# Performance work log

Hardware: AMD Instinct MI355X
Metric: run time of the kernel (lower is better)

Reference implementation:

```python
import jax, jax.numpy as jnp
import numpy as np

B, L, D = 2, 2048, 2048
H, G, E = 16, 4, 128       # num_heads, group_num, head dim
KV = H // G                # kv heads = 4
OUT = D                    # output_dim == input_dim for residual


def setup_inputs() -> dict:
    key = jax.random.key(0)
    ks = jax.random.split(key, 12)
    s_in = 1.0 / np.sqrt(D)
    s_o = 1.0 / np.sqrt(H * E)
    return {
        "x": jax.random.normal(ks[0], (B, L, D), jnp.float32),
        "Wq": jax.random.normal(ks[1], (D, H * E), jnp.float32) * s_in,
        "bq": jnp.zeros((H * E,), jnp.float32),
        "Wk": jax.random.normal(ks[2], (D, KV * E), jnp.float32) * s_in,
        "bk": jnp.zeros((KV * E,), jnp.float32),
        "Wv": jax.random.normal(ks[3], (D, KV * E), jnp.float32) * s_in,
        "bv": jnp.zeros((KV * E,), jnp.float32),
        "Wo": jax.random.normal(ks[4], (H * E, OUT), jnp.float32) * s_o,
        "bo": jnp.zeros((OUT,), jnp.float32),
        "gamma": jnp.ones((OUT,), jnp.float32),
        "beta": jnp.zeros((OUT,), jnp.float32),
    }


def reference(x, Wq, bq, Wk, bk, Wv, bv, Wo, bo, gamma, beta):
    b, l, _ = x.shape
    Q = (x @ Wq + bq).reshape(b, l, H, E)            # [B,L,H,E]
    K = (x @ Wk + bk).reshape(b, l, KV, E)           # [B,L,KV,E]
    V = (x @ Wv + bv).reshape(b, l, KV, E)
    # GQA expand: reshape(B,L,1,KV,E).expand(G) -> head h = g*KV + kv (tile kv heads G times)
    K = jnp.broadcast_to(K[:, :, None, :, :], (b, l, G, KV, E)).reshape(b, l, H, E)
    V = jnp.broadcast_to(V[:, :, None, :, :], (b, l, G, KV, E)).reshape(b, l, H, E)
    scores = jnp.einsum('blhe,bmhe->bhlm', Q, K) / np.sqrt(E).astype(np.float32)
    # causal mask: triu(ones, diag=1) * -1e9 added to scores
    mask = jnp.triu(jnp.ones((l, l), jnp.float32), k=1) * (-1e9)
    attn = jax.nn.softmax(scores + mask[None, None, :, :], axis=-1)
    ctx = jnp.einsum('bhlm,bmhe->blhe', attn, V).reshape(b, l, H * E)
    y = jax.nn.gelu(ctx @ Wo + bo, approximate=False)  # nn.GELU default = exact erf
    r = x + y
    mu = jnp.mean(r, axis=-1, keepdims=True)
    var = jnp.var(r, axis=-1, keepdims=True)
    return (r - mu) * jax.lax.rsqrt(var + 1e-5) * gamma + beta
```

## Files before the change

### kernel.cpp

```cpp
#include <hip/hip_runtime.h>
#include <hip/hip_bf16.h>
#include <math.h>

typedef __bf16 bf16_t;
typedef __bf16 bf16x4 __attribute__((ext_vector_type(4)));
typedef __bf16 bf16x8 __attribute__((ext_vector_type(8)));
typedef float  f32x4  __attribute__((ext_vector_type(4)));
typedef float  f32x16 __attribute__((ext_vector_type(16)));

#define MFMA16(a,b,c) __builtin_amdgcn_mfma_f32_16x16x32_bf16((a),(b),(c),0,0,0)
#define MFMA32(a,b,c) __builtin_amdgcn_mfma_f32_32x32x16_bf16((a),(b),(c),0,0,0)

#define B_ 2
#define L_ 2048
#define D_ 2048
#define H_ 16
#define KV_ 4
#define E_ 128
#define M_ (B_*L_)
#define NQKV_ 3072

__device__ __forceinline__ void async_ld16(const bf16_t* g, bf16_t* l) {
    __builtin_amdgcn_global_load_lds((const __attribute__((address_space(1))) void*)g,
                                     (__attribute__((address_space(3))) void*)l, 16, 0, 0);
}

__global__ __launch_bounds__(256) void cast_bias_kernel(const float* __restrict__ src,
                                                        bf16_t* __restrict__ dst,
                                                        const float* __restrict__ bq,
                                                        const float* __restrict__ bk,
                                                        const float* __restrict__ bv,
                                                        float* __restrict__ qbias) {
    int bid = blockIdx.x;
    if (bid < 8192) {
        int i = (bid * 256 + threadIdx.x) * 4;
        float4 v = *(const float4*)(src + i);
        bf16x4 o;
        o.x = (bf16_t)v.x; o.y = (bf16_t)v.y; o.z = (bf16_t)v.z; o.w = (bf16_t)v.w;
        *(bf16x4*)(dst + i) = o;
    } else {
        int i = (bid - 8192) * 256 + threadIdx.x;
        if (i < 2048) qbias[i] = bq[i];
        else if (i < 2560) qbias[i] = bk[i - 2048];
        else if (i < 3072) qbias[i] = bv[i - 2560];
    }
}

__global__ __launch_bounds__(256) void wtrans_kernel(const float* __restrict__ Wq,
                                                     const float* __restrict__ Wk,
                                                     const float* __restrict__ Wv,
                                                     const float* __restrict__ Wo,
                                                     bf16_t* __restrict__ WqkvT,
                                                     bf16_t* __restrict__ WoT) {
    __shared__ float tile[32][33];
    int bx = blockIdx.x;
    const float* W; bf16_t* WT; int N, n0;
    if (bx < 64)      { W = Wq; WT = WqkvT;                  N = 2048; n0 = bx * 32; }
    else if (bx < 80) { W = Wk; WT = WqkvT + 2048 * 2048;    N = 512;  n0 = (bx - 64) * 32; }
    else if (bx < 96) { W = Wv; WT = WqkvT + 2560 * 2048;    N = 512;  n0 = (bx - 80) * 32; }
    else              { W = Wo; WT = WoT;                    N = 2048; n0 = (bx - 96) * 32; }
    int k0 = blockIdx.y * 32;
    int tx = threadIdx.x, ty = threadIdx.y;
    #pragma unroll
    for (int i = 0; i < 32; i += 8)
        tile[ty + i][tx] = W[(size_t)(k0 + ty + i) * N + n0 + tx];
    __syncthreads();
    #pragma unroll
    for (int i = 0; i < 32; i += 8)
        WT[(size_t)(n0 + ty + i) * 2048 + k0 + tx] = (bf16_t)tile[tx][ty + i];
}

__global__ __launch_bounds__(256) void transpose_v_kernel(const bf16_t* __restrict__ QKV,
                                                          bf16_t* __restrict__ Vt) {
    __shared__ bf16_t tile[32][33];
    int e0 = blockIdx.x * 32, l0 = blockIdx.y * 32;
    int bk = blockIdx.z;
    int b = bk >> 2, kv = bk & 3;
    int tx = threadIdx.x, ty = threadIdx.y;
    #pragma unroll
    for (int i = 0; i < 32; i += 8)
        tile[ty + i][tx] = QKV[(size_t)(b * L_ + l0 + ty + i) * NQKV_ + 2560 + kv * 128 + e0 + tx];
    __syncthreads();
    #pragma unroll
    for (int i = 0; i < 32; i += 8)
        Vt[((size_t)bk * 128 + e0 + ty + i) * L_ + l0 + tx] = tile[tx][ty + i];
}

template <bool OUT_BF16, bool GELU>
__global__ __launch_bounds__(256) void gemm_kernel(const bf16_t* __restrict__ A,
                                                   const bf16_t* __restrict__ BT,
                                                   const float* __restrict__ bias,
                                                   void* __restrict__ C,
                                                   int M, int N, int K) {
    __shared__ __align__(16) bf16_t sA[128][32];
    __shared__ __align__(16) bf16_t sB[128][32];
    int tid = threadIdx.x;
    int wave = tid >> 6, lane = tid & 63;
    int l16 = lane & 15, quad = lane >> 4;
    int row0 = blockIdx.y * 128;
    int col0 = blockIdx.x * 128;
    int wm = (wave >> 1) * 64;
    int wn = (wave & 1) * 64;

    f32x4 acc[4][4];
    #pragma unroll
    for (int i = 0; i < 4; ++i)
        #pragma unroll
        for (int j = 0; j < 4; ++j)
            acc[i][j] = f32x4{0.f, 0.f, 0.f, 0.f};

    for (int k0 = 0; k0 < K; k0 += 32) {
        #pragma unroll
        for (int c = 0; c < 2; ++c) {
            int lin = (c * 256 + tid) * 8;
            int r = lin >> 5, col = lin & 31;
            async_ld16(&A[(size_t)(row0 + r) * K + k0 + col], &sA[r][col]);
            async_ld16(&BT[(size_t)(col0 + r) * K + k0 + col], &sB[r][col]);
        }
        __syncthreads();
        bf16x8 af[4], bf[4];
        #pragma unroll
        for (int mt = 0; mt < 4; ++mt) af[mt] = *(const bf16x8*)&sA[wm + mt * 16 + l16][quad * 8];
        #pragma unroll
        for (int nt = 0; nt < 4; ++nt) bf[nt] = *(const bf16x8*)&sB[wn + nt * 16 + l16][quad * 8];
        #pragma unroll
        for (int mt = 0; mt < 4; ++mt)
            #pragma unroll
            for (int nt = 0; nt < 4; ++nt)
                acc[mt][nt] = MFMA16(af[mt], bf[nt], acc[mt][nt]);
        __syncthreads();
    }

    #pragma unroll
    for (int mt = 0; mt < 4; ++mt) {
        #pragma unroll
        for (int nt = 0; nt < 4; ++nt) {
            int gcol = col0 + wn + nt * 16 + l16;
            float bv = bias[gcol];
            #pragma unroll
            for (int r = 0; r < 4; ++r) {
                int grow = row0 + wm + mt * 16 + quad * 4 + r;
                float v = acc[mt][nt][r] + bv;
                if (GELU) v = 0.5f * v * (1.f + erff(v * 0.70710678118654752f));
                if (OUT_BF16) ((bf16_t*)C)[(size_t)grow * N + gcol] = (bf16_t)v;
                else          ((float*)C)[(size_t)grow * N + gcol] = v;
            }
        }
    }
}

__global__ __launch_bounds__(128, 2) void attn_kernel(const bf16_t* __restrict__ QKV,
                                                      const bf16_t* __restrict__ Vt,
                                                      bf16_t* __restrict__ Ctx) {
    __shared__ __align__(16) bf16_t sK[2][64][128];

    const int tid = threadIdx.x;
    const int wave = tid >> 6, lane = tid & 63;
    const int l31 = lane & 31, half = lane >> 5;

    const int idx = blockIdx.x;
    const int rr = idx >> 5;
    const int bh = idx & 31;
    const int u = (rr < 8) ? 31 - rr : (rr < 16) ? rr - 8 : (rr < 24) ? 39 - rr : rr - 16;
    const int h = bh & 15, b = bh >> 4;
    const int kv = h & 3;

    const bf16_t* Kbase = QKV + (size_t)b * L_ * NQKV_ + 2048 + kv * 128;
    const bf16_t* Vbase = Vt + (size_t)(b * 4 + kv) * 128 * L_;
    const float SC = 0.12754995f;

    const int qrow = u * 64 + wave * 32 + l31;

    bf16x8 qf[8];
    const bf16_t* Qrow = QKV + (size_t)(b * L_ + qrow) * NQKV_ + h * 128 + half * 8;
    #pragma unroll
    for (int et = 0; et < 8; ++et) qf[et] = *(const bf16x8*)&Qrow[et * 16];

    f32x16 acc[4];
    #pragma unroll
    for (int em = 0; em < 4; ++em)
        #pragma unroll
        for (int j = 0; j < 16; ++j) acc[em][j] = 0.f;
    float l_i = 0.f;

    #define STAGE_K(KT, BUF)                                                          \
        {                                                                             \
            int kk = (KT) * 64;                                                       \
            _Pragma("unroll")                                                         \
            for (int rep = 0; rep < 8; ++rep) {                                       \
                int ch = rep * 128 + tid;                                             \
                int rk = ch >> 4;                                                     \
                int sc = (ch & 15) ^ (rk & 15);                                       \
                async_ld16(&Kbase[(size_t)(kk + rk) * NQKV_ + sc * 8],                \
                           ((bf16_t*)sK[BUF]) + (size_t)ch * 8);                      \
            }                                                                         \
        }

    STAGE_K(0, 0);
    __syncthreads();

    for (int kt = 0; kt <= u; ++kt) {
        const int bufi = kt & 1;
        if (kt < u) STAGE_K(kt + 1, bufi ^ 1);

        bf16x8 vr[16];
        #pragma unroll
        for (int kc = 0; kc < 2; ++kc)
            #pragma unroll
            for (int em = 0; em < 4; ++em)
                vr[kc * 4 + em] = *(const bf16x8*)&Vbase[(size_t)(em * 32 + l31) * L_ +
                                                         kt * 64 + (kc * 2 + half) * 8];

        f32x16 s[2];
        #pragma unroll
        for (int mt = 0; mt < 2; ++mt)
            #pragma unroll
            for (int j = 0; j < 16; ++j) s[mt][j] = 0.f;
        __builtin_amdgcn_s_setprio(1);
        #pragma unroll
        for (int mt = 0; mt < 2; ++mt)
            #pragma unroll
            for (int et = 0; et < 8; ++et) {
                bf16x8 kf = *(const bf16x8*)&sK[bufi][mt * 32 + l31][((et * 2 + half) ^ (l31 & 15)) * 8];
                s[mt] = MFMA32(kf, qf[et], s[mt]);
            }
        __builtin_amdgcn_s_setprio(0);

        #pragma unroll
        for (int kc = 2; kc < 4; ++kc)
            #pragma unroll
            for (int em = 0; em < 4; ++em)
                vr[kc * 4 + em] = *(const bf16x8*)&Vbase[(size_t)(em * 32 + l31) * L_ +
                                                         kt * 64 + (kc * 2 + half) * 8];

        if (kt == u) {
            #pragma unroll
            for (int mt = 0; mt < 2; ++mt)
                #pragma unroll
                for (int j = 0; j < 16; ++j) {
                    int kidx = kt * 64 + mt * 32 + (j & 3) + 8 * (j >> 2) + 4 * half;
                    if (kidx > qrow) s[mt][j] = -3.0e38f;
                }
        }

        float rs = 0.f;
        #pragma unroll
        for (int mt = 0; mt < 2; ++mt)
            #pragma unroll
            for (int j = 0; j < 16; ++j) {
                float p = exp2f(s[mt][j] * SC);
                s[mt][j] = p;
                rs += p;
            }
        rs += __shfl_xor(rs, 32, 64);
        l_i += rs;

        bf16x4 pk[2][4];
        #pragma unroll
        for (int mt = 0; mt < 2; ++mt)
            #pragma unroll
            for (int g = 0; g < 4; ++g) {
                bf16x4 tt;
                #pragma unroll
                for (int i = 0; i < 4; ++i) tt[i] = (bf16_t)s[mt][g * 4 + i];
                pk[mt][g] = tt;
            }

        #pragma unroll
        for (int kc = 0; kc < 4; ++kc) {
            const int mts = kc >> 1, g0 = 2 * (kc & 1);
            bf16x4 send = half ? pk[mts][g0] : pk[mts][g0 + 1];
            bf16x4 keep = half ? pk[mts][g0 + 1] : pk[mts][g0];
            union { bf16x4 v; int i[2]; } su, ru;
            su.v = send;
            ru.i[0] = __shfl_xor(su.i[0], 32, 64);
            ru.i[1] = __shfl_xor(su.i[1], 32, 64);
            bf16x4 lo = half ? ru.v : keep;
            bf16x4 hi = half ? keep : ru.v;
            bf16x8 pf = __builtin_shufflevector(lo, hi, 0, 1, 2, 3, 4, 5, 6, 7);
            __builtin_amdgcn_s_setprio(1);
            #pragma unroll
            for (int em = 0; em < 4; ++em)
                acc[em] = MFMA32(vr[kc * 4 + em], pf, acc[em]);
            __builtin_amdgcn_s_setprio(0);
        }

        __syncthreads();
    }

    const float inv = 1.f / l_i;
    bf16_t* Cp = Ctx + (size_t)(b * L_ + qrow) * 2048 + h * 128;
    #pragma unroll
    for (int em = 0; em < 4; ++em)
        #pragma unroll
        for (int g = 0; g < 4; ++g) {
            bf16x4 ov;
            #pragma unroll
            for (int i = 0; i < 4; ++i) ov[i] = (bf16_t)(acc[em][g * 4 + i] * inv);
            *(bf16x4*)&Cp[em * 32 + g * 8 + half * 4] = ov;
        }
}

__global__ __launch_bounds__(256) void ln_kernel(const bf16_t* __restrict__ Y,
                                                 const float* __restrict__ X,
                                                 const float* __restrict__ gamma,
                                                 const float* __restrict__ beta,
                                                 float* __restrict__ out) {
    __shared__ float sr[2048];
    __shared__ float wred[8];
    size_t row = blockIdx.x;
    const bf16_t* y = Y + row * 2048;
    const float* x = X + row * 2048;
    float sum = 0.f, ssq = 0.f;
    #pragma unroll
    for (int c = 0; c < 2; ++c) {
        int i = (c * 256 + threadIdx.x) * 4;
        bf16x4 yv = *(const bf16x4*)(y + i);
        float4 xv = *(const float4*)(x + i);
        float r0 = xv.x + (float)yv[0];
        float r1 = xv.y + (float)yv[1];
        float r2 = xv.z + (float)yv[2];
        float r3 = xv.w + (float)yv[3];
        sr[i] = r0; sr[i + 1] = r1; sr[i + 2] = r2; sr[i + 3] = r3;
        sum += r0 + r1 + r2 + r3;
        ssq += r0 * r0 + r1 * r1 + r2 * r2 + r3 * r3;
    }
    #pragma unroll
    for (int off = 32; off > 0; off >>= 1) {
        sum += __shfl_xor(sum, off, 64);
        ssq += __shfl_xor(ssq, off, 64);
    }
    int wv = threadIdx.x >> 6;
    if ((threadIdx.x & 63) == 0) { wred[wv] = sum; wred[wv + 4] = ssq; }
    __syncthreads();
    sum = wred[0] + wred[1] + wred[2] + wred[3];
    ssq = wred[4] + wred[5] + wred[6] + wred[7];
    float mu = sum * (1.f / 2048.f);
    float var = ssq * (1.f / 2048.f) - mu * mu;
    float rstd = rsqrtf(var + 1e-5f);
    #pragma unroll
    for (int c = 0; c < 2; ++c) {
        int i = (c * 256 + threadIdx.x) * 4;
        float4 gv = *(const float4*)(gamma + i);
        float4 bv = *(const float4*)(beta + i);
        float4 o;
        o.x = (sr[i]     - mu) * rstd * gv.x + bv.x;
        o.y = (sr[i + 1] - mu) * rstd * gv.y + bv.y;
        o.z = (sr[i + 2] - mu) * rstd * gv.z + bv.z;
        o.w = (sr[i + 3] - mu) * rstd * gv.w + bv.w;
        *(float4*)(out + row * 2048 + i) = o;
    }
}

extern "C" void kernel_launch(void* const* d_in, const int* in_sizes, int n_in,
                              void* d_out, int out_size, void* d_ws, size_t ws_size,
                              hipStream_t stream) {
    const float* x     = (const float*)d_in[0];
    const float* Wq    = (const float*)d_in[1];
    const float* bq    = (const float*)d_in[2];
    const float* Wk    = (const float*)d_in[3];
    const float* bk    = (const float*)d_in[4];
    const float* Wv    = (const float*)d_in[5];
    const float* bv    = (const float*)d_in[6];
    const float* Wo    = (const float*)d_in[7];
    const float* bo    = (const float*)d_in[8];
    const float* gamma = (const float*)d_in[9];
    const float* beta  = (const float*)d_in[10];
    float* out = (float*)d_out;

    char* ws = (char*)d_ws;
    size_t off = 0;
    bf16_t* xb    = (bf16_t*)(ws + off); off += 16777216;
    bf16_t* WqkvT = (bf16_t*)(ws + off); off += 12582912;
    bf16_t* WoT   = (bf16_t*)(ws + off); off += 8388608;
    float*  qbias = (float*)(ws + off);  off += 12288;
    bf16_t* QKV   = (bf16_t*)(ws + off); off += 25165824;
    bf16_t* Vt    = (bf16_t*)(ws + off); off += 4194304;
    bf16_t* Cb    = (bf16_t*)(ws + off); off += 16777216;
    bf16_t* Yb    = (bf16_t*)(ws + off); off += 16777216;

    cast_bias_kernel<<<8204, 256, 0, stream>>>(x, xb, bq, bk, bv, qbias);
    wtrans_kernel<<<dim3(160, 64), dim3(32, 8), 0, stream>>>(Wq, Wk, Wv, Wo, WqkvT, WoT);

    gemm_kernel<true, false><<<dim3(24, 32), 256, 0, stream>>>(xb, WqkvT, qbias, QKV, M_, NQKV_, D_);
    transpose_v_kernel<<<dim3(4, 64, 8), dim3(32, 8), 0, stream>>>(QKV, Vt);
    attn_kernel<<<1024, 128, 0, stream>>>(QKV, Vt, Cb);
    gemm_kernel<true, true><<<dim3(16, 32), 256, 0, stream>>>(Cb, WoT, bo, Yb, M_, D_, 2048);
    ln_kernel<<<M_, 256, 0, stream>>>(Yb, x, gamma, beta, out);
}
```

Measured before the change: 358.7 us.

## Split attention KV loop across two wave pairs and merge partials via LDS

The attention block grows to 256 threads. Two wave pairs process alternating 64-key tiles for the same 64 query rows, each with its own double-buffered K staging. Their unnormalized accumulators and row sums are combined through shared memory at the end. This works because the softmax has no running max, so the partials can simply be added. The block order becomes a plain longest-first schedule, exp2f becomes the hardware intrinsic, and the row sum is split into four partial sums. The aim is to shorten the serial KV loop per block and improve latency hiding, at the cost of more LDS, a final reduction step, and idle waves on odd tile counts.

```diff
diff --git a/kernel.cpp b/kernel.cpp
--- a/kernel.cpp
+++ b/kernel.cpp
@@ -149,19 +149,20 @@
     }
 }
 
-__global__ __launch_bounds__(128, 2) void attn_kernel(const bf16_t* __restrict__ QKV,
+__global__ __launch_bounds__(256, 2) void attn_kernel(const bf16_t* __restrict__ QKV,
                                                       const bf16_t* __restrict__ Vt,
                                                       bf16_t* __restrict__ Ctx) {
-    __shared__ __align__(16) bf16_t sK[2][64][128];
+    __shared__ __align__(16) bf16_t sK[2][2][64][128];
 
     const int tid = threadIdx.x;
     const int wave = tid >> 6, lane = tid & 63;
     const int l31 = lane & 31, half = lane >> 5;
+    const int pair = wave >> 1, wv = wave & 1;
+    const int t127 = tid & 127;
 
     const int idx = blockIdx.x;
-    const int rr = idx >> 5;
+    const int u = 31 - (idx >> 5);
     const int bh = idx & 31;
-    const int u = (rr < 8) ? 31 - rr : (rr < 16) ? rr - 8 : (rr < 24) ? 39 - rr : rr - 16;
     const int h = bh & 15, b = bh >> 4;
     const int kv = h & 3;
 
@@ -169,7 +170,7 @@
     const bf16_t* Vbase = Vt + (size_t)(b * 4 + kv) * 128 * L_;
     const float SC = 0.12754995f;
 
-    const int qrow = u * 64 + wave * 32 + l31;
+    const int qrow = u * 64 + wv * 32 + l31;
 
     bf16x8 qf[8];
     const bf16_t* Qrow = QKV + (size_t)(b * L_ + qrow) * NQKV_ + h * 128 + half * 8;
@@ -188,104 +189,133 @@
             int kk = (KT) * 64;                                                       \
             _Pragma("unroll")                                                         \
             for (int rep = 0; rep < 8; ++rep) {                                       \
-                int ch = rep * 128 + tid;                                             \
+                int ch = rep * 128 + t127;                                            \
                 int rk = ch >> 4;                                                     \
                 int sc = (ch & 15) ^ (rk & 15);                                       \
                 async_ld16(&Kbase[(size_t)(kk + rk) * NQKV_ + sc * 8],                \
-                           ((bf16_t*)sK[BUF]) + (size_t)ch * 8);                      \
+                           ((bf16_t*)sK[pair][BUF]) + (size_t)ch * 8);                \
             }                                                                         \
         }
 
-    STAGE_K(0, 0);
+    if (pair <= u) STAGE_K(pair, 0);
     __syncthreads();
 
-    for (int kt = 0; kt <= u; ++kt) {
-        const int bufi = kt & 1;
-        if (kt < u) STAGE_K(kt + 1, bufi ^ 1);
-
-        bf16x8 vr[16];
-        #pragma unroll
-        for (int kc = 0; kc < 2; ++kc)
-            #pragma unroll
-            for (int em = 0; em < 4; ++em)
-                vr[kc * 4 + em] = *(const bf16x8*)&Vbase[(size_t)(em * 32 + l31) * L_ +
-                                                         kt * 64 + (kc * 2 + half) * 8];
-
-        f32x16 s[2];
-        #pragma unroll
-        for (int mt = 0; mt < 2; ++mt)
-            #pragma unroll
-            for (int j = 0; j < 16; ++j) s[mt][j] = 0.f;
-        __builtin_amdgcn_s_setprio(1);
-        #pragma unroll
-        for (int mt = 0; mt < 2; ++mt)
-            #pragma unroll
-            for (int et = 0; et < 8; ++et) {
-                bf16x8 kf = *(const bf16x8*)&sK[bufi][mt * 32 + l31][((et * 2 + half) ^ (l31 & 15)) * 8];
-                s[mt] = MFMA32(kf, qf[et], s[mt]);
+    const int J = (u >> 1) + 1;
+    for (int j = 0; j < J; ++j) {
+        const int kt = 2 * j + pair;
+        const int bufi = j & 1;
+        const bool active = (kt <= u);
+        if (kt + 2 <= u) STAGE_K(kt + 2, bufi ^ 1);
+
+        if (active) {
+            bf16x8 vr[16];
+            #pragma unroll
+            for (int kc = 0; kc < 2; ++kc)
+                #pragma unroll
+                for (int em = 0; em < 4; ++em)
+                    vr[kc * 4 + em] = *(const bf16x8*)&Vbase[(size_t)(em * 32 + l31) * L_ +
+                                                             kt * 64 + (kc * 2 + half) * 8];
+
+            f32x16 s[2];
+            #pragma unroll
+            for (int mt = 0; mt < 2; ++mt)
+                #pragma unroll
+                for (int jj = 0; jj < 16; ++jj) s[mt][jj] = 0.f;
+            __builtin_amdgcn_s_setprio(1);
+            #pragma unroll
+            for (int mt = 0; mt < 2; ++mt)
+                #pragma unroll
+                for (int et = 0; et < 8; ++et) {
+                    bf16x8 kf = *(const bf16x8*)&sK[pair][bufi][mt * 32 + l31][((et * 2 + half) ^ (l31 & 15)) * 8];
+                    s[mt] = MFMA32(kf, qf[et], s[mt]);
+                }
+            __builtin_amdgcn_s_setprio(0);
+
+            #pragma unroll
+            for (int kc = 2; kc < 4; ++kc)
+                #pragma unroll
+                for (int em = 0; em < 4; ++em)
+                    vr[kc * 4 + em] = *(const bf16x8*)&Vbase[(size_t)(em * 32 + l31) * L_ +
+                                                             kt * 64 + (kc * 2 + half) * 8];
+
+            if (kt == u) {
+                #pragma unroll
+                for (int mt = 0; mt < 2; ++mt)
+                    #pragma unroll
+                    for (int jj = 0; jj < 16; ++jj) {
+                        int kidx = kt * 64 + mt * 32 + (jj & 3) + 8 * (jj >> 2) + 4 * half;
+                        if (kidx > qrow) s[mt][jj] = -3.0e38f;
+                    }
             }
-        __builtin_amdgcn_s_setprio(0);
-
-        #pragma unroll
-        for (int kc = 2; kc < 4; ++kc)
-            #pragma unroll
-            for (int em = 0; em < 4; ++em)
-                vr[kc * 4 + em] = *(const bf16x8*)&Vbase[(size_t)(em * 32 + l31) * L_ +
-                                                         kt * 64 + (kc * 2 + half) * 8];
-
-        if (kt == u) {
+
+            float rs0 = 0.f, rs1 = 0.f, rs2 = 0.f, rs3 = 0.f;
             #pragma unroll
             for (int mt = 0; mt < 2; ++mt)
                 #pragma unroll
-                for (int j = 0; j < 16; ++j) {
-                    int kidx = kt * 64 + mt * 32 + (j & 3) + 8 * (j >> 2) + 4 * half;
-                    if (kidx > qrow) s[mt][j] = -3.0e38f;
+                for (int jj = 0; jj < 16; ++jj) {
+                    float p = __builtin_amdgcn_exp2f(s[mt][jj] * SC);
+                    s[mt][jj] = p;
+                    if ((jj & 3) == 0) rs0 += p;
+                    else if ((jj & 3) == 1) rs1 += p;
+                    else if ((jj & 3) == 2) rs2 += p;
+                    else rs3 += p;
                 }
+            float rs = (rs0 + rs1) + (rs2 + rs3);
+            rs += __shfl_xor(rs, 32, 64);
+            l_i += rs;
+
+            bf16x4 pk[2][4];
+            #pragma unroll
+            for (int mt = 0; mt < 2; ++mt)
+                #pragma unroll
+                for (int g = 0; g < 4; ++g) {
+                    bf16x4 tt;
+                    #pragma unroll
+                    for (int i = 0; i < 4; ++i) tt[i] = (bf16_t)s[mt][g * 4 + i];
+                    pk[mt][g] = tt;
+                }
+
+            #pragma unroll
+            for (int kc = 0; kc < 4; ++kc) {
+                const int mts = kc >> 1, g0 = 2 * (kc & 1);
+                bf16x4 send = half ? pk[mts][g0] : pk[mts][g0 + 1];
+                bf16x4 keep = half ? pk[mts][g0 + 1] : pk[mts][g0];
+                union { bf16x4 v; int i[2]; } su, ru;
+                su.v = send;
+                ru.i[0] = __shfl_xor(su.i[0], 32, 64);
+                ru.i[1] = __shfl_xor(su.i[1], 32, 64);
+                bf16x4 lo = half ? ru.v : keep;
+                bf16x4 hi = half ? keep : ru.v;
+                bf16x8 pf = __builtin_shufflevector(lo, hi, 0, 1, 2, 3, 4, 5, 6, 7);
+                __builtin_amdgcn_s_setprio(1);
+                #pragma unroll
+                for (int em = 0; em < 4; ++em)
+                    acc[em] = MFMA32(vr[kc * 4 + em], pf, acc[em]);
+                __builtin_amdgcn_s_setprio(0);
+            }
         }
 
-        float rs = 0.f;
-        #pragma unroll
-        for (int mt = 0; mt < 2; ++mt)
-            #pragma unroll
-            for (int j = 0; j < 16; ++j) {
-                float p = exp2f(s[mt][j] * SC);
-                s[mt][j] = p;
-                rs += p;
-            }
-        rs += __shfl_xor(rs, 32, 64);
-        l_i += rs;
-
-        bf16x4 pk[2][4];
-        #pragma unroll
-        for (int mt = 0; mt < 2; ++mt)
-            #pragma unroll
-            for (int g = 0; g < 4; ++g) {
-                bf16x4 tt;
-                #pragma unroll
-                for (int i = 0; i < 4; ++i) tt[i] = (bf16_t)s[mt][g * 4 + i];
-                pk[mt][g] = tt;
-            }
-
-        #pragma unroll
-        for (int kc = 0; kc < 4; ++kc) {
-            const int mts = kc >> 1, g0 = 2 * (kc & 1);
-            bf16x4 send = half ? pk[mts][g0] : pk[mts][g0 + 1];
-            bf16x4 keep = half ? pk[mts][g0 + 1] : pk[mts][g0];
-            union { bf16x4 v; int i[2]; } su, ru;
-            su.v = send;
-            ru.i[0] = __shfl_xor(su.i[0], 32, 64);
-            ru.i[1] = __shfl_xor(su.i[1], 32, 64);
-            bf16x4 lo = half ? ru.v : keep;
-            bf16x4 hi = half ? keep : ru.v;
-            bf16x8 pf = __builtin_shufflevector(lo, hi, 0, 1, 2, 3, 4, 5, 6, 7);
-            __builtin_amdgcn_s_setprio(1);
-            #pragma unroll
-            for (int em = 0; em < 4; ++em)
-                acc[em] = MFMA32(vr[kc * 4 + em], pf, acc[em]);
-            __builtin_amdgcn_s_setprio(0);
-        }
-
         __syncthreads();
+    }
+
+    float* cl = (float*)sK;
+    if (pair == 1) {
+        float* p = cl + (size_t)(wv * 64 + lane) * 65;
+        #pragma unroll
+        for (int em = 0; em < 4; ++em)
+            #pragma unroll
+            for (int r = 0; r < 16; ++r) p[em * 16 + r] = acc[em][r];
+        p[64] = l_i;
+    }
+    __syncthreads();
+    if (pair == 1) return;
+    {
+        const float* p = cl + (size_t)(wv * 64 + lane) * 65;
+        #pragma unroll
+        for (int em = 0; em < 4; ++em)
+            #pragma unroll
+            for (int r = 0; r < 16; ++r) acc[em][r] += p[em * 16 + r];
+        l_i += p[64];
     }
 
     const float inv = 1.f / l_i;
@@ -384,7 +414,7 @@
 
     gemm_kernel<true, false><<<dim3(24, 32), 256, 0, stream>>>(xb, WqkvT, qbias, QKV, M_, NQKV_, D_);
     transpose_v_kernel<<<dim3(4, 64, 8), dim3(32, 8), 0, stream>>>(QKV, Vt);
-    attn_kernel<<<1024, 128, 0, stream>>>(QKV, Vt, Cb);
+    attn_kernel<<<1024, 256, 0, stream>>>(QKV, Vt, Cb);
     gemm_kernel<true, true><<<dim3(16, 32), 256, 0, stream>>>(Cb, WoT, bo, Yb, M_, D_, 2048);
     ln_kernel<<<M_, 256, 0, stream>>>(Yb, x, gamma, beta, out);
 }
```

New measurement: 364.1 us. Within noise of the previous version (+1.5%).

## Fuse V transpose into QKV GEMM epilogue, swizzle GEMM block order, hoist V loads

Applied to the files above, without the earlier changes.

The QKV GEMM epilogue now writes the V columns straight into the transposed Vt layout with 4-wide bf16 stores, so the separate transpose_v kernel and its extra pass over V are removed. Both GEMMs also remap block indices into 8 interleaved groups, aiming for better L2/MALL locality across concurrently running tiles. In the attention loop, all 16 V fragment loads are now issued before the QK MFMAs rather than split around them. This raises register pressure in the attention kernel and may lose some latency hiding.

```diff
diff --git a/kernel.cpp b/kernel.cpp
--- a/kernel.cpp
+++ b/kernel.cpp
@@ -70,35 +70,23 @@
         WT[(size_t)(n0 + ty + i) * 2048 + k0 + tx] = (bf16_t)tile[tx][ty + i];
 }
 
-__global__ __launch_bounds__(256) void transpose_v_kernel(const bf16_t* __restrict__ QKV,
-                                                          bf16_t* __restrict__ Vt) {
-    __shared__ bf16_t tile[32][33];
-    int e0 = blockIdx.x * 32, l0 = blockIdx.y * 32;
-    int bk = blockIdx.z;
-    int b = bk >> 2, kv = bk & 3;
-    int tx = threadIdx.x, ty = threadIdx.y;
-    #pragma unroll
-    for (int i = 0; i < 32; i += 8)
-        tile[ty + i][tx] = QKV[(size_t)(b * L_ + l0 + ty + i) * NQKV_ + 2560 + kv * 128 + e0 + tx];
-    __syncthreads();
-    #pragma unroll
-    for (int i = 0; i < 32; i += 8)
-        Vt[((size_t)bk * 128 + e0 + ty + i) * L_ + l0 + tx] = tile[tx][ty + i];
-}
-
-template <bool OUT_BF16, bool GELU>
+template <bool OUT_BF16, bool GELU, bool VSPLIT>
 __global__ __launch_bounds__(256) void gemm_kernel(const bf16_t* __restrict__ A,
                                                    const bf16_t* __restrict__ BT,
                                                    const float* __restrict__ bias,
                                                    void* __restrict__ C,
+                                                   bf16_t* __restrict__ Vt,
                                                    int M, int N, int K) {
     __shared__ __align__(16) bf16_t sA[128][32];
     __shared__ __align__(16) bf16_t sB[128][32];
     int tid = threadIdx.x;
     int wave = tid >> 6, lane = tid & 63;
     int l16 = lane & 15, quad = lane >> 4;
-    int row0 = blockIdx.y * 128;
-    int col0 = blockIdx.x * 128;
+    int flat = blockIdx.y * gridDim.x + blockIdx.x;
+    int cpx = (gridDim.x * gridDim.y) >> 3;
+    int swz = (flat & 7) * cpx + (flat >> 3);
+    int col0 = (swz % gridDim.x) * 128;
+    int row0 = (swz / gridDim.x) * 128;
     int wm = (wave >> 1) * 64;
     int wn = (wave & 1) * 64;
 
@@ -137,13 +125,26 @@
         for (int nt = 0; nt < 4; ++nt) {
             int gcol = col0 + wn + nt * 16 + l16;
             float bv = bias[gcol];
+            float vv[4];
             #pragma unroll
             for (int r = 0; r < 4; ++r) {
-                int grow = row0 + wm + mt * 16 + quad * 4 + r;
                 float v = acc[mt][nt][r] + bv;
                 if (GELU) v = 0.5f * v * (1.f + erff(v * 0.70710678118654752f));
-                if (OUT_BF16) ((bf16_t*)C)[(size_t)grow * N + gcol] = (bf16_t)v;
-                else          ((float*)C)[(size_t)grow * N + gcol] = v;
+                vv[r] = v;
+            }
+            int grow0 = row0 + wm + mt * 16 + quad * 4;
+            if (VSPLIT && gcol >= 2560) {
+                int b = grow0 >> 11, l = grow0 & 2047;
+                bf16x4 ov;
+                #pragma unroll
+                for (int r = 0; r < 4; ++r) ov[r] = (bf16_t)vv[r];
+                *(bf16x4*)&Vt[((size_t)(b * 512) + (gcol - 2560)) * L_ + l] = ov;
+            } else {
+                #pragma unroll
+                for (int r = 0; r < 4; ++r) {
+                    if (OUT_BF16) ((bf16_t*)C)[(size_t)(grow0 + r) * N + gcol] = (bf16_t)vv[r];
+                    else          ((float*)C)[(size_t)(grow0 + r) * N + gcol] = vv[r];
+                }
             }
         }
     }
@@ -205,7 +206,7 @@
 
         bf16x8 vr[16];
         #pragma unroll
-        for (int kc = 0; kc < 2; ++kc)
+        for (int kc = 0; kc < 4; ++kc)
             #pragma unroll
             for (int em = 0; em < 4; ++em)
                 vr[kc * 4 + em] = *(const bf16x8*)&Vbase[(size_t)(em * 32 + l31) * L_ +
@@ -225,13 +226,6 @@
                 s[mt] = MFMA32(kf, qf[et], s[mt]);
             }
         __builtin_amdgcn_s_setprio(0);
-
-        #pragma unroll
-        for (int kc = 2; kc < 4; ++kc)
-            #pragma unroll
-            for (int em = 0; em < 4; ++em)
-                vr[kc * 4 + em] = *(const bf16x8*)&Vbase[(size_t)(em * 32 + l31) * L_ +
-                                                         kt * 64 + (kc * 2 + half) * 8];
 
         if (kt == u) {
             #pragma unroll
@@ -382,9 +376,8 @@
     cast_bias_kernel<<<8204, 256, 0, stream>>>(x, xb, bq, bk, bv, qbias);
     wtrans_kernel<<<dim3(160, 64), dim3(32, 8), 0, stream>>>(Wq, Wk, Wv, Wo, WqkvT, WoT);
 
-    gemm_kernel<true, false><<<dim3(24, 32), 256, 0, stream>>>(xb, WqkvT, qbias, QKV, M_, NQKV_, D_);
-    transpose_v_kernel<<<dim3(4, 64, 8), dim3(32, 8), 0, stream>>>(QKV, Vt);
+    gemm_kernel<true, false, true><<<dim3(24, 32), 256, 0, stream>>>(xb, WqkvT, qbias, QKV, Vt, M_, NQKV_, D_);
     attn_kernel<<<1024, 128, 0, stream>>>(QKV, Vt, Cb);
-    gemm_kernel<true, true><<<dim3(16, 32), 256, 0, stream>>>(Cb, WoT, bo, Yb, M_, D_, 2048);
+    gemm_kernel<true, true, false><<<dim3(16, 32), 256, 0, stream>>>(Cb, WoT, bo, Yb, nullptr, M_, D_, 2048);
     ln_kernel<<<M_, 256, 0, stream>>>(Yb, x, gamma, beta, out);
 }
```

After: 352.1 us. Within noise of the previous version (-1.9%).
